# Performance work log

Hardware: AMD Instinct MI355X
Metric: run time of the kernel (lower is better)

## Reference

```python
import jax, jax.numpy as jnp
import numpy as np

B, S, HID, NH, INTER, VOCAB = 8, 1024, 512, 8, 2048, 30522
EPS = 1e-12


def _layernorm(x, w, b):
    m = jnp.mean(x, axis=-1, keepdims=True)
    v = jnp.mean((x - m) ** 2, axis=-1, keepdims=True)
    return (x - m) * jax.lax.rsqrt(v + EPS) * w + b


def _multihead_mut(x, M):
    # x: (b, s, d); M: (H, s, s). Split d into H heads, mix along the
    # sequence axis per head: out[b,t,h,d] = sum_s x[b,s,h,d] * M[h,s,t]
    b, s, d = x.shape
    xh = x.reshape(b, s, NH, d // NH)
    out = jnp.einsum('bshd,hst->bthd', xh, M)
    return out.reshape(b, s, d)


def setup_inputs() -> dict:
    key = jax.random.key(0)
    ks = jax.random.split(key, 14)
    g = lambda i, shape, scale: jax.random.normal(ks[i], shape, dtype=jnp.float32) * scale
    return {
        'x': jax.random.randint(ks[0], (B, S), 0, VOCAB),
        'word_emb': g(1, (VOCAB, HID), 0.02),
        'pos_emb': g(2, (S, HID), 0.02),
        'tok_emb': g(3, (2, HID), 0.02),
        'emb_ln_w': jnp.ones((HID,), dtype=jnp.float32),
        'emb_ln_b': jnp.zeros((HID,), dtype=jnp.float32),
        'init_d': g(4, (INTER, HID), 0.02),
        'init_b': g(5, (INTER,), 0.02),
        'init_M': g(6, (NH, S, S), 1.0 / np.sqrt(S)),
        'inter0_d': g(7, (INTER, INTER), 1.0 / np.sqrt(INTER)),
        'inter0_b': g(8, (INTER,), 0.02),
        'inter0_M': g(9, (NH, S, S), 1.0 / np.sqrt(S)),
        'final_d': g(10, (HID, INTER), 1.0 / np.sqrt(INTER)),
        'final_b': g(11, (HID,), 0.02),
    }


def reference(x, word_emb, pos_emb, tok_emb, emb_ln_w, emb_ln_b,
              init_d, init_b, init_M, inter0_d, inter0_b, inter0_M,
              final_d, final_b):
    # BertEmbeddings: word + position + token_type(all zeros) -> LayerNorm
    emb = word_emb[x] + pos_emb[None, :, :] + tok_emb[0][None, None, :]
    xo = _layernorm(emb, emb_ln_w, emb_ln_b)  # (B, S, HID)

    # layer 0 (flattened): project to intermediate, per-head seq mix, bias, quad act
    xo = xo @ init_d.T                      # (B, S, INTER)
    xo = _multihead_mut(xo, init_M)
    xo = xo + init_b
    xo = xo * xo                            # activation_quad

    # layer 1 (flattened)
    xo = xo @ inter0_d.T                    # (B, S, INTER)
    xo = _multihead_mut(xo, inter0_M)
    xo = xo + inter0_b
    xo = xo * xo                            # activation_quad

    return xo @ final_d.T + final_b         # (B, S, HID)
```

## Files before the change

### kernel.cpp

```cpp
#include <hip/hip_runtime.h>

typedef _Float16 f16;
typedef _Float16 f16x4 __attribute__((ext_vector_type(4)));
typedef _Float16 f16x8 __attribute__((ext_vector_type(8)));
typedef float    f32x4 __attribute__((ext_vector_type(4)));

#define SEQ   1024
#define HID   512
#define NHEAD 8
#define DH    256
#define INTER 2048
#define BATCH 8
#define ROWS  (BATCH * SEQ)

__device__ __forceinline__ void mm_core(const f16* __restrict__ At,
                                        const f16* __restrict__ Bt,
                                        int K, f32x4 (&acc)[4][4]) {
  __shared__ __align__(16) f16 As[2 * 4096];
  __shared__ __align__(16) f16 Bs[2 * 4096];
  const int tid  = threadIdx.x;
  const int lane = tid & 63, wv = tid >> 6;
  const int wm = (wv >> 1) * 64, wn = (wv & 1) * 64;
  const int lrow  = lane & 15;
  const int kfrag = (lane >> 4) * 8;
  const int c1 = wv * 64 + lane;
  const int r1 = c1 >> 2, kq1 = (c1 & 3) * 8;
  const int r2 = r1 + 64;
  const int e1 = r1 * 32 + (kq1 ^ (((r1 >> 1) & 3) << 3));
  const int e2 = r2 * 32 + (kq1 ^ (((r2 >> 1) & 3) << 3));
  const f16* Ap1 = At + (size_t)r1 * K + kq1;
  const f16* Ap2 = At + (size_t)r2 * K + kq1;
  const f16* Bp1 = Bt + (size_t)r1 * K + kq1;
  const f16* Bp2 = Bt + (size_t)r2 * K + kq1;
  int4 ra1 = *(const int4*)Ap1;
  int4 ra2 = *(const int4*)Ap2;
  int4 rb1 = *(const int4*)Bp1;
  int4 rb2 = *(const int4*)Bp2;
  *(int4*)&As[e1] = ra1;
  *(int4*)&As[e2] = ra2;
  *(int4*)&Bs[e1] = rb1;
  *(int4*)&Bs[e2] = rb2;
  if (K > 32) {
    ra1 = *(const int4*)(Ap1 + 32);
    ra2 = *(const int4*)(Ap2 + 32);
    rb1 = *(const int4*)(Bp1 + 32);
    rb2 = *(const int4*)(Bp2 + 32);
  }
  int aoff[4], boff[4];
  #pragma unroll
  for (int t = 0; t < 4; ++t) {
    int ra = wm + t * 16 + lrow;
    aoff[t] = ra * 32 + (kfrag ^ (((ra >> 1) & 3) << 3));
    int rb = wn + t * 16 + lrow;
    boff[t] = rb * 32 + (kfrag ^ (((rb >> 1) & 3) << 3));
  }
  __syncthreads();
  int cur = 0;
  for (int k0 = 0; k0 < K; k0 += 32) {
    const int nxt = (cur ^ 1) * 4096;
    if (k0 + 32 < K) {
      *(int4*)&As[nxt + e1] = ra1;
      *(int4*)&As[nxt + e2] = ra2;
      *(int4*)&Bs[nxt + e1] = rb1;
      *(int4*)&Bs[nxt + e2] = rb2;
      if (k0 + 64 < K) {
        ra1 = *(const int4*)(Ap1 + k0 + 64);
        ra2 = *(const int4*)(Ap2 + k0 + 64);
        rb1 = *(const int4*)(Bp1 + k0 + 64);
        rb2 = *(const int4*)(Bp2 + k0 + 64);
      }
    }
    const int cb = cur * 4096;
    f16x8 af[4], bf[4];
    #pragma unroll
    for (int t = 0; t < 4; ++t) {
      af[t] = *(const f16x8*)&As[cb + aoff[t]];
      bf[t] = *(const f16x8*)&Bs[cb + boff[t]];
    }
    #pragma unroll
    for (int i = 0; i < 4; ++i)
      #pragma unroll
      for (int j = 0; j < 4; ++j)
        acc[i][j] = __builtin_amdgcn_mfma_f32_16x16x32_f16(af[i], bf[j],
                                                           acc[i][j], 0, 0, 0);
    __syncthreads();
    cur ^= 1;
  }
}

__device__ __forceinline__ void zero_acc(f32x4 (&acc)[4][4]) {
  f32x4 z = {0.f, 0.f, 0.f, 0.f};
  #pragma unroll
  for (int i = 0; i < 4; ++i)
    #pragma unroll
    for (int j = 0; j < 4; ++j) acc[i][j] = z;
}

__global__ __launch_bounds__(256) void gemm_t_kernel(
    const f16* __restrict__ A, const f16* __restrict__ W,
    f16* __restrict__ Xt, int K) {
  int row0 = blockIdx.y * 128, col0 = blockIdx.x * 128;
  f32x4 acc[4][4];
  zero_acc(acc);
  mm_core(A + (size_t)row0 * K, W + (size_t)col0 * K, K, acc);
  int tid = threadIdx.x, lane = tid & 63, wv = tid >> 6;
  int wm = (wv >> 1) * 64, wn = (wv & 1) * 64;
  int cn = lane & 15, rbase = (lane >> 4) * 4;
  int b = row0 >> 10, sbase = row0 & 1023;
  #pragma unroll
  for (int mt = 0; mt < 4; ++mt) {
    int s = sbase + wm + mt * 16 + rbase;
    #pragma unroll
    for (int nt = 0; nt < 4; ++nt) {
      int n = col0 + wn + nt * 16 + cn;
      int h = n >> 8, d = n & 255;
      f16x4 v = {(f16)acc[mt][nt][0], (f16)acc[mt][nt][1],
                 (f16)acc[mt][nt][2], (f16)acc[mt][nt][3]};
      *(f16x4*)&Xt[(((size_t)(b * 8 + h) * 256 + d) << 10) + s] = v;
    }
  }
}

__global__ __launch_bounds__(256) void mut_kernel(
    const f16* __restrict__ Mt, const f16* __restrict__ Xt,
    const float* __restrict__ bias, f16* __restrict__ Y) {
  int b = blockIdx.z >> 3, h = blockIdx.z & 7;
  int t0 = blockIdx.y * 128, d0 = blockIdx.x * 128;
  f32x4 acc[4][4];
  zero_acc(acc);
  const f16* Ap = Mt + ((size_t)h << 20) + ((size_t)t0 << 10);
  const f16* Bp = Xt + (((size_t)(b * 8 + h) * 256 + d0) << 10);
  mm_core(Ap, Bp, SEQ, acc);
  int tid = threadIdx.x, lane = tid & 63, wv = tid >> 6;
  int wm = (wv >> 1) * 64, wn = (wv & 1) * 64;
  int cn = lane & 15, rbase = (lane >> 4) * 4;
  #pragma unroll
  for (int mt = 0; mt < 4; ++mt) {
    int t = t0 + wm + mt * 16 + rbase;
    #pragma unroll
    for (int nt = 0; nt < 4; ++nt) {
      int d = d0 + wn + nt * 16 + cn;
      float bb = bias[(h << 8) + d];
      size_t base = (((size_t)(b << 10) + t) << 11) + (h << 8) + d;
      #pragma unroll
      for (int r = 0; r < 4; ++r) {
        float v = acc[mt][nt][r] + bb;
        Y[base + (size_t)r * INTER] = (f16)(v * v);
      }
    }
  }
}

__global__ __launch_bounds__(256) void gemm_out_kernel(
    const f16* __restrict__ A, const f16* __restrict__ W,
    const float* __restrict__ bias, float* __restrict__ out, int K, int N) {
  int row0 = blockIdx.y * 128, col0 = blockIdx.x * 128;
  f32x4 acc[4][4];
  zero_acc(acc);
  mm_core(A + (size_t)row0 * K, W + (size_t)col0 * K, K, acc);
  int tid = threadIdx.x, lane = tid & 63, wv = tid >> 6;
  int wm = (wv >> 1) * 64, wn = (wv & 1) * 64;
  int cn = lane & 15, rbase = (lane >> 4) * 4;
  #pragma unroll
  for (int mt = 0; mt < 4; ++mt) {
    int r0 = row0 + wm + mt * 16 + rbase;
    #pragma unroll
    for (int nt = 0; nt < 4; ++nt) {
      int col = col0 + wn + nt * 16 + cn;
      float bb = bias[col];
      #pragma unroll
      for (int r = 0; r < 4; ++r)
        out[(size_t)(r0 + r) * N + col] = acc[mt][nt][r] + bb;
    }
  }
}

__global__ __launch_bounds__(256) void embed_ln_kernel(
    const int* __restrict__ x, const float* __restrict__ wemb,
    const float* __restrict__ pemb, const float* __restrict__ temb,
    const float* __restrict__ lnw, const float* __restrict__ lnb,
    f16* __restrict__ out) {
  int row = blockIdx.x;
  int s = row & (SEQ - 1);
  int tok = x[row];
  const float* we = wemb + (size_t)tok * HID;
  const float* pe = pemb + (size_t)s * HID;
  int c = threadIdx.x;
  float e0 = we[c] + pe[c] + temb[c];
  float e1 = we[c + 256] + pe[c + 256] + temb[c + 256];
  float s1 = e0 + e1, s2 = e0 * e0 + e1 * e1;
  #pragma unroll
  for (int off = 32; off > 0; off >>= 1) {
    s1 += __shfl_down(s1, off, 64);
    s2 += __shfl_down(s2, off, 64);
  }
  __shared__ float r1[4], r2[4];
  int wid = threadIdx.x >> 6, lane = threadIdx.x & 63;
  if (lane == 0) { r1[wid] = s1; r2[wid] = s2; }
  __syncthreads();
  float S1 = r1[0] + r1[1] + r1[2] + r1[3];
  float S2 = r2[0] + r2[1] + r2[2] + r2[3];
  float m = S1 * (1.0f / HID);
  float v = S2 * (1.0f / HID) - m * m;
  float inv = rsqrtf(v + 1e-12f);
  f16* o = out + (size_t)row * HID;
  o[c]       = (f16)((e0 - m) * inv * lnw[c]       + lnb[c]);
  o[c + 256] = (f16)((e1 - m) * inv * lnw[c + 256] + lnb[c + 256]);
}

__global__ __launch_bounds__(256) void cast_f16_kernel(
    const float* __restrict__ in, f16* __restrict__ out, int n) {
  int i = (blockIdx.x * 256 + threadIdx.x) * 4;
  if (i < n) {
    float4 v = *(const float4*)(in + i);
    f16x4 o = {(f16)v.x, (f16)v.y, (f16)v.z, (f16)v.w};
    *(f16x4*)(out + i) = o;
  }
}

__global__ __launch_bounds__(256) void mtrans_kernel(
    const float* __restrict__ M, f16* __restrict__ Mt) {
  __shared__ float T[32][33];
  int h = blockIdx.z;
  int s0 = blockIdx.y * 32, t0 = blockIdx.x * 32;
  int tx = threadIdx.x & 31, ty = threadIdx.x >> 5;
  const float* Mh = M + ((size_t)h << 20);
  #pragma unroll
  for (int i = 0; i < 32; i += 8)
    T[ty + i][tx] = Mh[((size_t)(s0 + ty + i) << 10) + t0 + tx];
  __syncthreads();
  f16* Mth = Mt + ((size_t)h << 20);
  #pragma unroll
  for (int i = 0; i < 32; i += 8)
    Mth[((size_t)(t0 + ty + i) << 10) + s0 + tx] = (f16)T[tx][ty + i];
}

extern "C" void kernel_launch(void* const* d_in, const int* in_sizes, int n_in,
                              void* d_out, int out_size, void* d_ws, size_t ws_size,
                              hipStream_t stream) {
  const int*   x        = (const int*)d_in[0];
  const float* wemb     = (const float*)d_in[1];
  const float* pemb     = (const float*)d_in[2];
  const float* temb     = (const float*)d_in[3];
  const float* lnw      = (const float*)d_in[4];
  const float* lnb      = (const float*)d_in[5];
  const float* init_d   = (const float*)d_in[6];
  const float* init_b   = (const float*)d_in[7];
  const float* init_M   = (const float*)d_in[8];
  const float* inter0_d = (const float*)d_in[9];
  const float* inter0_b = (const float*)d_in[10];
  const float* inter0_M = (const float*)d_in[11];
  const float* final_d  = (const float*)d_in[12];
  const float* final_b  = (const float*)d_in[13];
  float* out = (float*)d_out;

  char* ws = (char*)d_ws;
  f16* R0 = (f16*)(ws);
  f16* R1 = (f16*)(ws + 8388608);
  f16* R2 = (f16*)(ws + 10485760);
  f16* R3 = (f16*)(ws + 27262976);
  f16* R4 = (f16*)(ws + 60817408);
  f16* R5 = (f16*)(ws + 94371840);

  embed_ln_kernel<<<ROWS, 256, 0, stream>>>(x, wemb, pemb, temb, lnw, lnb, R0);
  cast_f16_kernel<<<(INTER * HID / 4 + 255) / 256, 256, 0, stream>>>(init_d, R1, INTER * HID);
  mtrans_kernel<<<dim3(32, 32, 8), 256, 0, stream>>>(init_M, R2);
  gemm_t_kernel<<<dim3(INTER / 128, ROWS / 128), 256, 0, stream>>>(R0, R1, R3, HID);
  mut_kernel<<<dim3(DH / 128, SEQ / 128, BATCH * NHEAD), 256, 0, stream>>>(R2, R3, init_b, R4);
  cast_f16_kernel<<<(INTER * INTER / 4 + 255) / 256, 256, 0, stream>>>(inter0_d, R0, INTER * INTER);
  mtrans_kernel<<<dim3(32, 32, 8), 256, 0, stream>>>(inter0_M, R2);
  gemm_t_kernel<<<dim3(INTER / 128, ROWS / 128), 256, 0, stream>>>(R4, R0, R5, INTER);
  mut_kernel<<<dim3(DH / 128, SEQ / 128, BATCH * NHEAD), 256, 0, stream>>>(R2, R5, inter0_b, R3);
  cast_f16_kernel<<<(HID * INTER / 4 + 255) / 256, 256, 0, stream>>>(final_d, R1, HID * INTER);
  gemm_out_kernel<<<dim3(HID / 128, ROWS / 128), 256, 0, stream>>>(R3, R1, final_b, out, INTER, HID);
}
```

Before: 454.7 us.

## Split-K the final projection GEMM and merge the two M transposes

The final GEMM (N=512, K=2048) launched only 4x64 = 256 blocks. It now splits K into two halves with a z grid dimension, writes fp32 partials to workspace, and sums them with bias in a separate elementwise kernel. This is meant to roughly double the parallelism available on the GPU's compute units. Separately, the two mixing-matrix transposes are merged into one launch writing into two distinct buffers, which removes a launch and its serialization. The cost is an extra pass writing and reading 32 MB of fp32 partials.

```diff
diff --git a/kernel.cpp b/kernel.cpp
--- a/kernel.cpp
+++ b/kernel.cpp
@@ -15,7 +15,7 @@
 
 __device__ __forceinline__ void mm_core(const f16* __restrict__ At,
                                         const f16* __restrict__ Bt,
-                                        int K, f32x4 (&acc)[4][4]) {
+                                        int K, int ld, f32x4 (&acc)[4][4]) {
   __shared__ __align__(16) f16 As[2 * 4096];
   __shared__ __align__(16) f16 Bs[2 * 4096];
   const int tid  = threadIdx.x;
@@ -28,10 +28,10 @@
   const int r2 = r1 + 64;
   const int e1 = r1 * 32 + (kq1 ^ (((r1 >> 1) & 3) << 3));
   const int e2 = r2 * 32 + (kq1 ^ (((r2 >> 1) & 3) << 3));
-  const f16* Ap1 = At + (size_t)r1 * K + kq1;
-  const f16* Ap2 = At + (size_t)r2 * K + kq1;
-  const f16* Bp1 = Bt + (size_t)r1 * K + kq1;
-  const f16* Bp2 = Bt + (size_t)r2 * K + kq1;
+  const f16* Ap1 = At + (size_t)r1 * ld + kq1;
+  const f16* Ap2 = At + (size_t)r2 * ld + kq1;
+  const f16* Bp1 = Bt + (size_t)r1 * ld + kq1;
+  const f16* Bp2 = Bt + (size_t)r2 * ld + kq1;
   int4 ra1 = *(const int4*)Ap1;
   int4 ra2 = *(const int4*)Ap2;
   int4 rb1 = *(const int4*)Bp1;
@@ -102,7 +102,7 @@
   int row0 = blockIdx.y * 128, col0 = blockIdx.x * 128;
   f32x4 acc[4][4];
   zero_acc(acc);
-  mm_core(A + (size_t)row0 * K, W + (size_t)col0 * K, K, acc);
+  mm_core(A + (size_t)row0 * K, W + (size_t)col0 * K, K, K, acc);
   int tid = threadIdx.x, lane = tid & 63, wv = tid >> 6;
   int wm = (wv >> 1) * 64, wn = (wv & 1) * 64;
   int cn = lane & 15, rbase = (lane >> 4) * 4;
@@ -130,7 +130,7 @@
   zero_acc(acc);
   const f16* Ap = Mt + ((size_t)h << 20) + ((size_t)t0 << 10);
   const f16* Bp = Xt + (((size_t)(b * 8 + h) * 256 + d0) << 10);
-  mm_core(Ap, Bp, SEQ, acc);
+  mm_core(Ap, Bp, SEQ, SEQ, acc);
   int tid = threadIdx.x, lane = tid & 63, wv = tid >> 6;
   int wm = (wv >> 1) * 64, wn = (wv & 1) * 64;
   int cn = lane & 15, rbase = (lane >> 4) * 4;
@@ -151,13 +151,17 @@
   }
 }
 
-__global__ __launch_bounds__(256) void gemm_out_kernel(
+__global__ __launch_bounds__(256) void gemm_splitk_kernel(
     const f16* __restrict__ A, const f16* __restrict__ W,
-    const float* __restrict__ bias, float* __restrict__ out, int K, int N) {
+    float* __restrict__ partials) {
   int row0 = blockIdx.y * 128, col0 = blockIdx.x * 128;
+  int z = blockIdx.z;
+  int koff = z * 1024;
+  float* P = partials + (size_t)z * ROWS * HID;
   f32x4 acc[4][4];
   zero_acc(acc);
-  mm_core(A + (size_t)row0 * K, W + (size_t)col0 * K, K, acc);
+  mm_core(A + (size_t)row0 * INTER + koff,
+          W + (size_t)col0 * INTER + koff, 1024, INTER, acc);
   int tid = threadIdx.x, lane = tid & 63, wv = tid >> 6;
   int wm = (wv >> 1) * 64, wn = (wv & 1) * 64;
   int cn = lane & 15, rbase = (lane >> 4) * 4;
@@ -167,12 +171,22 @@
     #pragma unroll
     for (int nt = 0; nt < 4; ++nt) {
       int col = col0 + wn + nt * 16 + cn;
-      float bb = bias[col];
       #pragma unroll
       for (int r = 0; r < 4; ++r)
-        out[(size_t)(r0 + r) * N + col] = acc[mt][nt][r] + bb;
-    }
-  }
+        P[(size_t)(r0 + r) * HID + col] = acc[mt][nt][r];
+    }
+  }
+}
+
+__global__ __launch_bounds__(256) void addbias_kernel(
+    const float* __restrict__ p0, const float* __restrict__ p1,
+    const float* __restrict__ bias, float* __restrict__ out) {
+  int i = (blockIdx.x * 256 + threadIdx.x) * 4;
+  float4 a = *(const float4*)(p0 + i);
+  float4 b = *(const float4*)(p1 + i);
+  float4 c = *(const float4*)(bias + (i & (HID - 1)));
+  *(float4*)(out + i) = make_float4(a.x + b.x + c.x, a.y + b.y + c.y,
+                                    a.z + b.z + c.z, a.w + b.w + c.w);
 }
 
 __global__ __launch_bounds__(256) void embed_ln_kernel(
@@ -218,18 +232,20 @@
   }
 }
 
-__global__ __launch_bounds__(256) void mtrans_kernel(
-    const float* __restrict__ M, f16* __restrict__ Mt) {
+__global__ __launch_bounds__(256) void mtrans2_kernel(
+    const float* __restrict__ M1, const float* __restrict__ M2,
+    f16* __restrict__ Mt1, f16* __restrict__ Mt2) {
   __shared__ float T[32][33];
-  int h = blockIdx.z;
+  int z = blockIdx.z;
+  int h = z & 7;
+  const float* Mh = (z < 8 ? M1 : M2) + ((size_t)h << 20);
+  f16* Mth = (z < 8 ? Mt1 : Mt2) + ((size_t)h << 20);
   int s0 = blockIdx.y * 32, t0 = blockIdx.x * 32;
   int tx = threadIdx.x & 31, ty = threadIdx.x >> 5;
-  const float* Mh = M + ((size_t)h << 20);
   #pragma unroll
   for (int i = 0; i < 32; i += 8)
     T[ty + i][tx] = Mh[((size_t)(s0 + ty + i) << 10) + t0 + tx];
   __syncthreads();
-  f16* Mth = Mt + ((size_t)h << 20);
   #pragma unroll
   for (int i = 0; i < 32; i += 8)
     Mth[((size_t)(t0 + ty + i) << 10) + s0 + tx] = (f16)T[tx][ty + i];
@@ -255,22 +271,25 @@
   float* out = (float*)d_out;
 
   char* ws = (char*)d_ws;
-  f16* R0 = (f16*)(ws);
-  f16* R1 = (f16*)(ws + 8388608);
-  f16* R2 = (f16*)(ws + 10485760);
-  f16* R3 = (f16*)(ws + 27262976);
-  f16* R4 = (f16*)(ws + 60817408);
-  f16* R5 = (f16*)(ws + 94371840);
+  f16*   R0  = (f16*)(ws);
+  f16*   R1  = (f16*)(ws + 8388608);
+  f16*   Mt1 = (f16*)(ws + 10485760);
+  f16*   Mt2 = (f16*)(ws + 27262976);
+  f16*   R3  = (f16*)(ws + 44040192);
+  f16*   R4  = (f16*)(ws + 77594624);
+  f16*   R5  = (f16*)(ws + 111149056);
+  float* Pp  = (float*)R5;
 
   embed_ln_kernel<<<ROWS, 256, 0, stream>>>(x, wemb, pemb, temb, lnw, lnb, R0);
   cast_f16_kernel<<<(INTER * HID / 4 + 255) / 256, 256, 0, stream>>>(init_d, R1, INTER * HID);
-  mtrans_kernel<<<dim3(32, 32, 8), 256, 0, stream>>>(init_M, R2);
+  mtrans2_kernel<<<dim3(32, 32, 16), 256, 0, stream>>>(init_M, inter0_M, Mt1, Mt2);
   gemm_t_kernel<<<dim3(INTER / 128, ROWS / 128), 256, 0, stream>>>(R0, R1, R3, HID);
-  mut_kernel<<<dim3(DH / 128, SEQ / 128, BATCH * NHEAD), 256, 0, stream>>>(R2, R3, init_b, R4);
+  mut_kernel<<<dim3(DH / 128, SEQ / 128, BATCH * NHEAD), 256, 0, stream>>>(Mt1, R3, init_b, R4);
   cast_f16_kernel<<<(INTER * INTER / 4 + 255) / 256, 256, 0, stream>>>(inter0_d, R0, INTER * INTER);
-  mtrans_kernel<<<dim3(32, 32, 8), 256, 0, stream>>>(inter0_M, R2);
   gemm_t_kernel<<<dim3(INTER / 128, ROWS / 128), 256, 0, stream>>>(R4, R0, R5, INTER);
-  mut_kernel<<<dim3(DH / 128, SEQ / 128, BATCH * NHEAD), 256, 0, stream>>>(R2, R5, inter0_b, R3);
+  mut_kernel<<<dim3(DH / 128, SEQ / 128, BATCH * NHEAD), 256, 0, stream>>>(Mt2, R5, inter0_b, R3);
   cast_f16_kernel<<<(HID * INTER / 4 + 255) / 256, 256, 0, stream>>>(final_d, R1, HID * INTER);
-  gemm_out_kernel<<<dim3(HID / 128, ROWS / 128), 256, 0, stream>>>(R3, R1, final_b, out, INTER, HID);
-}
+  gemm_splitk_kernel<<<dim3(HID / 128, ROWS / 128, 2), 256, 0, stream>>>(R3, R1, Pp);
+  addbias_kernel<<<ROWS * HID / 1024, 256, 0, stream>>>(
+      Pp, Pp + (size_t)ROWS * HID, final_b, out);
+}
```

Result: slower. 470.1 us (+3.4%).
